# Optimization experiments

Hardware: AMD Instinct MI355X
Metric: run time of the kernel (lower is better)

## Reference

```python
import jax, jax.numpy as jnp
import numpy as np

N_NODES = 50000
N_EDGES = 1600000


def setup_inputs() -> dict:
    key = jax.random.key(0)
    k1, k2, k3, k4 = jax.random.split(key, 4)
    x = jax.random.normal(k1, (N_NODES, 256), dtype=jnp.float32)
    edge_index = jax.random.randint(k2, (2, N_EDGES), 0, N_NODES, dtype=jnp.int64)
    W1 = jax.random.normal(k3, (256, 128), dtype=jnp.float32) * 0.05
    b1 = jnp.zeros((128,), dtype=jnp.float32)
    Wc = jax.random.normal(k4, (128, 10), dtype=jnp.float32) * 0.05
    bc = jnp.zeros((10,), dtype=jnp.float32)
    return {"x": x, "edge_index": edge_index, "W1": W1, "b1": b1,
            "Wc": Wc, "bc": bc, "conv_time": 30}


def reference(x, edge_index, W1, b1, Wc, bc, conv_time):
    """GCNConv(num_features->nhid) with conv_time propagation hops, ReLU, Linear cls."""
    n = x.shape[0]
    # linear transform first (standard GCNConv: transform then propagate)
    h = x @ W1 + b1  # [N, nhid]
    # add self-loops (GCN default)
    loop = jnp.arange(n, dtype=edge_index.dtype)
    src = jnp.concatenate([edge_index[0], loop])
    dst = jnp.concatenate([edge_index[1], loop])
    # symmetric normalization D^{-1/2} A_hat D^{-1/2}
    deg = jax.ops.segment_sum(jnp.ones_like(dst, dtype=h.dtype), dst, num_segments=n)
    dinv = jax.lax.rsqrt(jnp.maximum(deg, 1.0))
    norm = (dinv[src] * dinv[dst])[:, None]  # [E+N, 1]

    def hop(i, h):
        msg = h[src] * norm                      # gather + scale
        return jax.ops.segment_sum(msg, dst, num_segments=n)  # scatter-add

    h = jax.lax.fori_loop(0, conv_time, hop, h)
    h = jax.nn.relu(h)
    return h @ Wc + bc  # [N, num_classes]
```

## Files before the change

### kernel.cpp

```cpp
#include <hip/hip_runtime.h>
#include <hip/hip_bf16.h>

#define NFEAT 256
#define NHID  128
#define NCLS  10
#define CONV_TIME 30
#define NSLICE 8
#define SFEAT  16

__global__ void deg_kernel(const int* __restrict__ ei, int* __restrict__ cnt, int E) {
    int e = blockIdx.x * blockDim.x + threadIdx.x;
    if (e < E) {
        int d = ei[(size_t)E + e];
        atomicAdd(&cnt[d], 1);
    }
}

__global__ void dinv_kernel(const int* __restrict__ cnt, float* __restrict__ dinv, int n) {
    int i = blockIdx.x * blockDim.x + threadIdx.x;
    if (i < n) {
        float deg = (float)(cnt[i] + 1);
        dinv[i] = 1.0f / sqrtf(deg);
    }
}

__global__ void scan_kernel(const int* __restrict__ cnt, int* __restrict__ offs,
                            int* __restrict__ pos, int n) {
    __shared__ int lds[256];
    int tid = threadIdx.x;
    int per = (n + 255) >> 8;
    int beg = tid * per;
    int end = min(beg + per, n);
    int sum = 0;
    for (int i = beg; i < end; ++i) sum += cnt[i];
    lds[tid] = sum;
    __syncthreads();
    if (tid == 0) {
        int acc = 0;
        for (int i = 0; i < 256; ++i) { int t = lds[i]; lds[i] = acc; acc += t; }
    }
    __syncthreads();
    int run = lds[tid];
    for (int i = beg; i < end; ++i) { offs[i] = run; pos[i] = run; run += cnt[i]; }
    if (tid == 255) offs[n] = run;
}

__global__ void scatter_kernel(const int* __restrict__ ei, int* __restrict__ pos,
                               unsigned short* __restrict__ esrc, int E) {
    int e = blockIdx.x * blockDim.x + threadIdx.x;
    if (e < E) {
        int s = ei[e];
        int d = ei[(size_t)E + e];
        int p = atomicAdd(&pos[d], 1);
        esrc[p] = (unsigned short)s;
    }
}

__global__ void init_dummy_kernel(float* __restrict__ hA, float* __restrict__ hB,
                                  int n, int np1) {
    int t = threadIdx.x;
    if (t < NSLICE * SFEAT) {
        int sl = t >> 4, f = t & 15;
        size_t idx = (size_t)sl * np1 * SFEAT + (size_t)n * SFEAT + f;
        hA[idx] = 0.0f;
        hB[idx] = 0.0f;
    }
}

__global__ __launch_bounds__(256) void gemm1_kernel(const float* __restrict__ x,
                                                    const float* __restrict__ W1,
                                                    const float* __restrict__ b1,
                                                    const float* __restrict__ dinv,
                                                    float* __restrict__ g, int M, int np1) {
    __shared__ float As[64][20];
    __shared__ float Bs[16][128];
    int tid = threadIdx.x;
    int m0  = blockIdx.x * 64;
    int tx  = tid & 15;
    int ty  = tid >> 4;
    int ar  = tid >> 2, aq = tid & 3;
    int br  = tid >> 4, bc = tid & 15;

    float acc[4][8];
#pragma unroll
    for (int i = 0; i < 4; ++i)
#pragma unroll
        for (int j = 0; j < 8; ++j) acc[i][j] = 0.0f;

    for (int kb = 0; kb < NFEAT; kb += 16) {
        float4 av = make_float4(0.f, 0.f, 0.f, 0.f);
        int arow = m0 + ar;
        if (arow < M) av = *(const float4*)(x + (size_t)arow * NFEAT + kb + aq * 4);
        *(float4*)&As[ar][aq * 4] = av;
        *(float4*)&Bs[br][bc * 8]     = *(const float4*)(W1 + (size_t)(kb + br) * NHID + bc * 8);
        *(float4*)&Bs[br][bc * 8 + 4] = *(const float4*)(W1 + (size_t)(kb + br) * NHID + bc * 8 + 4);
        __syncthreads();
#pragma unroll
        for (int k = 0; k < 16; ++k) {
            float a0 = As[ty * 4 + 0][k];
            float a1 = As[ty * 4 + 1][k];
            float a2 = As[ty * 4 + 2][k];
            float a3 = As[ty * 4 + 3][k];
            float4 b0 = *(float4*)&Bs[k][tx * 8];
            float4 b1v = *(float4*)&Bs[k][tx * 8 + 4];
            float bv[8] = {b0.x, b0.y, b0.z, b0.w, b1v.x, b1v.y, b1v.z, b1v.w};
            float avv[4] = {a0, a1, a2, a3};
#pragma unroll
            for (int i = 0; i < 4; ++i)
#pragma unroll
                for (int j = 0; j < 8; ++j)
                    acc[i][j] = fmaf(avv[i], bv[j], acc[i][j]);
        }
        __syncthreads();
    }
    int col0 = tx * 8;
    int sl   = col0 >> 4;
    int c0   = col0 & 15;
#pragma unroll
    for (int i = 0; i < 4; ++i) {
        int row = m0 + ty * 4 + i;
        if (row < M) {
            float dv = dinv[row];
            float* dst = g + (size_t)sl * np1 * SFEAT + (size_t)row * SFEAT + c0;
#pragma unroll
            for (int j = 0; j < 8; ++j)
                dst[j] = dv * (acc[i][j] + b1[col0 + j]);
        }
    }
}

__global__ __launch_bounds__(256) void hop_kernel(const float* __restrict__ gin,
                                                  float* __restrict__ gout,
                                                  const int* __restrict__ offs,
                                                  const unsigned short* __restrict__ esrc,
                                                  const float* __restrict__ dinv,
                                                  int n, int np1, int last) {
    int bid  = blockIdx.x;
    int sl   = bid & (NSLICE - 1);
    int grp  = (bid >> 3) * 4 + (threadIdx.x >> 6);
    if (grp * 16 >= n) return;
    int lane = threadIdx.x & 63;
    int slot = lane >> 2;
    int fl   = lane & 3;
    int node = grp * 16 + slot;
    bool valid = node < n;
    int nodeC = valid ? node : n;
    const float4* __restrict__ gs4 = (const float4*)(gin + (size_t)sl * np1 * SFEAT);
    float4*       __restrict__ go4 = (float4*)(gout + (size_t)sl * np1 * SFEAT);

    int beg = 0, deg = 0;
    if (valid) { beg = offs[node]; deg = offs[node + 1] - beg; }
    int dmax = deg;
    dmax = max(dmax, __shfl_xor(dmax, 4, 64));
    dmax = max(dmax, __shfl_xor(dmax, 8, 64));
    dmax = max(dmax, __shfl_xor(dmax, 16, 64));
    dmax = max(dmax, __shfl_xor(dmax, 32, 64));

    float4 acc = make_float4(0.f, 0.f, 0.f, 0.f);
    int degm1 = (deg > 0) ? (deg - 1) : 0;
    for (int i = 0; i < dmax; i += 8) {
#pragma unroll
        for (int j = 0; j < 8; ++j) {
            int a   = beg + min(i + j, degm1);
            int src = (int)esrc[a];
            src     = (i + j < deg) ? src : n;
            float4 v = gs4[(size_t)src * 4 + fl];
            acc.x += v.x; acc.y += v.y; acc.z += v.z; acc.w += v.w;
        }
    }
    float4 sf = gs4[(size_t)nodeC * 4 + fl];
    acc.x += sf.x; acc.y += sf.y; acc.z += sf.z; acc.w += sf.w;
    float dv = valid ? dinv[node] : 1.0f;
    float sc = last ? dv : dv * dv;
    acc.x *= sc; acc.y *= sc; acc.z *= sc; acc.w *= sc;
    if (valid) go4[(size_t)node * 4 + fl] = acc;
}

__global__ __launch_bounds__(256) void cls_kernel(const float* __restrict__ h,
                                                  const float* __restrict__ Wc,
                                                  const float* __restrict__ bc,
                                                  float* __restrict__ out, int n, int np1) {
    __shared__ float wc[NHID * NCLS];
    __shared__ float bcs[NCLS];
    int tid = threadIdx.x;
    for (int i = tid; i < NHID * NCLS; i += 256) wc[i] = Wc[i];
    if (tid < NCLS) bcs[tid] = bc[tid];
    __syncthreads();
    int i = blockIdx.x * 256 + tid;
    if (i >= n) return;
    float acc[NCLS];
#pragma unroll
    for (int c = 0; c < NCLS; ++c) acc[c] = bcs[c];
#pragma unroll
    for (int s = 0; s < NSLICE; ++s) {
        const float4* hr = (const float4*)(h + ((size_t)s * np1 + i) * SFEAT);
#pragma unroll
        for (int q = 0; q < 4; ++q) {
            float4 v = hr[q];
            float vs[4] = {fmaxf(v.x, 0.f), fmaxf(v.y, 0.f), fmaxf(v.z, 0.f), fmaxf(v.w, 0.f)};
#pragma unroll
            for (int j = 0; j < 4; ++j)
#pragma unroll
                for (int c = 0; c < NCLS; ++c)
                    acc[c] = fmaf(vs[j], wc[(s * SFEAT + q * 4 + j) * NCLS + c], acc[c]);
        }
    }
#pragma unroll
    for (int c = 0; c < NCLS; ++c) out[(size_t)i * NCLS + c] = acc[c];
}

static inline size_t align256(size_t x) { return (x + 255) & ~(size_t)255; }

extern "C" void kernel_launch(void* const* d_in, const int* in_sizes, int n_in,
                              void* d_out, int out_size, void* d_ws, size_t ws_size,
                              hipStream_t stream) {
    const float* x   = (const float*)d_in[0];
    const int*   ei  = (const int*)d_in[1];
    const float* W1  = (const float*)d_in[2];
    const float* b1  = (const float*)d_in[3];
    const float* Wc  = (const float*)d_in[4];
    const float* bc  = (const float*)d_in[5];
    float*       out = (float*)d_out;

    const int N   = in_sizes[0] / NFEAT;
    const int E   = in_sizes[1] / 2;
    const int NP1 = N + 1;

    char* ws = (char*)d_ws;
    size_t off = 0;
    float*          hA   = (float*)(ws + off); off = align256(off + (size_t)NSLICE * NP1 * SFEAT * 4);
    float*          hB   = (float*)(ws + off); off = align256(off + (size_t)NSLICE * NP1 * SFEAT * 4);
    int*            cnt  = (int*)  (ws + off); off = align256(off + (size_t)N * 4);
    float*          dinv = (float*)(ws + off); off = align256(off + (size_t)N * 4);
    int*            offs = (int*)  (ws + off); off = align256(off + (size_t)(N + 1) * 4);
    int*            pos  = (int*)  (ws + off); off = align256(off + (size_t)N * 4);
    unsigned short* esrc = (unsigned short*)(ws + off); off = align256(off + ((size_t)E + 64) * 2);

    hipMemsetAsync(cnt, 0, (size_t)N * 4, stream);

    deg_kernel<<<(E + 255) / 256, 256, 0, stream>>>(ei, cnt, E);
    dinv_kernel<<<(N + 255) / 256, 256, 0, stream>>>(cnt, dinv, N);
    scan_kernel<<<1, 256, 0, stream>>>(cnt, offs, pos, N);
    scatter_kernel<<<(E + 255) / 256, 256, 0, stream>>>(ei, pos, esrc, E);
    init_dummy_kernel<<<1, 256, 0, stream>>>(hA, hB, N, NP1);

    gemm1_kernel<<<(N + 63) / 64, 256, 0, stream>>>(x, W1, b1, dinv, hA, N, NP1);

    int ngrp = (N + 15) / 16;
    int hop_blocks = NSLICE * ((ngrp + 3) / 4);
    for (int i = 0; i < CONV_TIME; ++i) {
        const float* gi = (i & 1) ? hB : hA;
        float*       go = (i & 1) ? hA : hB;
        hop_kernel<<<hop_blocks, 256, 0, stream>>>(gi, go, offs, esrc, dinv, N, NP1,
                                                   (i == CONV_TIME - 1) ? 1 : 0);
    }

    cls_kernel<<<(N + 255) / 256, 256, 0, stream>>>(hA, Wc, bc, out, N, NP1);
}
```

Baseline: 2.658 ms.

## Pad per-node edge lists to multiples of eight and load indices as uint4

```diff
diff --git a/kernel.cpp b/kernel.cpp
--- a/kernel.cpp
+++ b/kernel.cpp
@@ -24,25 +24,35 @@
     }
 }
 
-__global__ void scan_kernel(const int* __restrict__ cnt, int* __restrict__ offs,
-                            int* __restrict__ pos, int n) {
-    __shared__ int lds[256];
-    int tid = threadIdx.x;
-    int per = (n + 255) >> 8;
-    int beg = tid * per;
-    int end = min(beg + per, n);
-    int sum = 0;
-    for (int i = beg; i < end; ++i) sum += cnt[i];
-    lds[tid] = sum;
-    __syncthreads();
-    if (tid == 0) {
-        int acc = 0;
-        for (int i = 0; i < 256; ++i) { int t = lds[i]; lds[i] = acc; acc += t; }
-    }
-    __syncthreads();
-    int run = lds[tid];
-    for (int i = beg; i < end; ++i) { offs[i] = run; pos[i] = run; run += cnt[i]; }
-    if (tid == 255) offs[n] = run;
+__global__ void alloc_kernel(const int* __restrict__ cnt, int* __restrict__ alloc,
+                             int* __restrict__ pbeg, int* __restrict__ plen,
+                             int* __restrict__ pos, int n) {
+    int i    = blockIdx.x * blockDim.x + threadIdx.x;
+    int lane = threadIdx.x & 63;
+    int pl   = 0;
+    if (i < n) pl = (cnt[i] + 7) & ~7;
+    int v = pl;
+#pragma unroll
+    for (int d = 1; d < 64; d <<= 1) {
+        int t = __shfl_up(v, d, 64);
+        if (lane >= d) v += t;
+    }
+    int total = __shfl(v, 63, 64);
+    int excl  = v - pl;
+    int base  = 0;
+    if (lane == 63) base = atomicAdd(alloc, total);
+    base = __shfl(base, 63, 64);
+    if (i < n) {
+        int seg = base + excl;
+        pbeg[i] = seg;
+        plen[i] = pl;
+        pos[i]  = seg;
+    }
+}
+
+__global__ void fill_esrc_kernel(unsigned int* __restrict__ esrc32, unsigned int val, int nwords) {
+    int i = blockIdx.x * blockDim.x + threadIdx.x;
+    if (i < nwords) esrc32[i] = val;
 }
 
 __global__ void scatter_kernel(const int* __restrict__ ei, int* __restrict__ pos,
@@ -131,7 +141,8 @@
 
 __global__ __launch_bounds__(256) void hop_kernel(const float* __restrict__ gin,
                                                   float* __restrict__ gout,
-                                                  const int* __restrict__ offs,
+                                                  const int* __restrict__ pbeg,
+                                                  const int* __restrict__ plen,
                                                   const unsigned short* __restrict__ esrc,
                                                   const float* __restrict__ dinv,
                                                   int n, int np1, int last) {
@@ -148,25 +159,29 @@
     const float4* __restrict__ gs4 = (const float4*)(gin + (size_t)sl * np1 * SFEAT);
     float4*       __restrict__ go4 = (float4*)(gout + (size_t)sl * np1 * SFEAT);
 
-    int beg = 0, deg = 0;
-    if (valid) { beg = offs[node]; deg = offs[node + 1] - beg; }
-    int dmax = deg;
-    dmax = max(dmax, __shfl_xor(dmax, 4, 64));
-    dmax = max(dmax, __shfl_xor(dmax, 8, 64));
-    dmax = max(dmax, __shfl_xor(dmax, 16, 64));
-    dmax = max(dmax, __shfl_xor(dmax, 32, 64));
+    int beg = 0, L = 0;
+    if (valid) { beg = pbeg[node]; L = plen[node]; }
 
     float4 acc = make_float4(0.f, 0.f, 0.f, 0.f);
-    int degm1 = (deg > 0) ? (deg - 1) : 0;
-    for (int i = 0; i < dmax; i += 8) {
-#pragma unroll
-        for (int j = 0; j < 8; ++j) {
-            int a   = beg + min(i + j, degm1);
-            int src = (int)esrc[a];
-            src     = (i + j < deg) ? src : n;
-            float4 v = gs4[(size_t)src * 4 + fl];
-            acc.x += v.x; acc.y += v.y; acc.z += v.z; acc.w += v.w;
-        }
+    const uint4* __restrict__ e4 = (const uint4*)esrc;
+    for (int i = 0; i < L; i += 8) {
+        uint4 w = e4[(beg + i) >> 3];
+        int s0 = w.x & 0xFFFF, s1 = w.x >> 16;
+        int s2 = w.y & 0xFFFF, s3 = w.y >> 16;
+        int s4 = w.z & 0xFFFF, s5 = w.z >> 16;
+        int s6 = w.w & 0xFFFF, s7 = w.w >> 16;
+        float4 v0 = gs4[(size_t)s0 * 4 + fl];
+        float4 v1 = gs4[(size_t)s1 * 4 + fl];
+        float4 v2 = gs4[(size_t)s2 * 4 + fl];
+        float4 v3 = gs4[(size_t)s3 * 4 + fl];
+        float4 v4 = gs4[(size_t)s4 * 4 + fl];
+        float4 v5 = gs4[(size_t)s5 * 4 + fl];
+        float4 v6 = gs4[(size_t)s6 * 4 + fl];
+        float4 v7 = gs4[(size_t)s7 * 4 + fl];
+        acc.x += v0.x + v1.x + v2.x + v3.x + v4.x + v5.x + v6.x + v7.x;
+        acc.y += v0.y + v1.y + v2.y + v3.y + v4.y + v5.y + v6.y + v7.y;
+        acc.z += v0.z + v1.z + v2.z + v3.z + v4.z + v5.z + v6.z + v7.z;
+        acc.w += v0.w + v1.w + v2.w + v3.w + v4.w + v5.w + v6.w + v7.w;
     }
     float4 sf = gs4[(size_t)nodeC * 4 + fl];
     acc.x += sf.x; acc.y += sf.y; acc.z += sf.z; acc.w += sf.w;
@@ -222,25 +237,33 @@
     const float* bc  = (const float*)d_in[5];
     float*       out = (float*)d_out;
 
-    const int N   = in_sizes[0] / NFEAT;
-    const int E   = in_sizes[1] / 2;
-    const int NP1 = N + 1;
+    const int N    = in_sizes[0] / NFEAT;
+    const int E    = in_sizes[1] / 2;
+    const int NP1  = N + 1;
+    const int EPAD = E + 8 * N + 64;
 
     char* ws = (char*)d_ws;
     size_t off = 0;
     float*          hA   = (float*)(ws + off); off = align256(off + (size_t)NSLICE * NP1 * SFEAT * 4);
     float*          hB   = (float*)(ws + off); off = align256(off + (size_t)NSLICE * NP1 * SFEAT * 4);
-    int*            cnt  = (int*)  (ws + off); off = align256(off + (size_t)N * 4);
+    int*            cnt  = (int*)  (ws + off); off = align256(off + (size_t)(N + 64) * 4);
     float*          dinv = (float*)(ws + off); off = align256(off + (size_t)N * 4);
-    int*            offs = (int*)  (ws + off); off = align256(off + (size_t)(N + 1) * 4);
+    int*            pbeg = (int*)  (ws + off); off = align256(off + (size_t)N * 4);
+    int*            plen = (int*)  (ws + off); off = align256(off + (size_t)N * 4);
     int*            pos  = (int*)  (ws + off); off = align256(off + (size_t)N * 4);
-    unsigned short* esrc = (unsigned short*)(ws + off); off = align256(off + ((size_t)E + 64) * 2);
-
-    hipMemsetAsync(cnt, 0, (size_t)N * 4, stream);
+    unsigned short* esrc = (unsigned short*)(ws + off); off = align256(off + (size_t)EPAD * 2);
+    int*            alloc = cnt + N;
+
+    hipMemsetAsync(cnt, 0, (size_t)(N + 64) * 4, stream);
 
     deg_kernel<<<(E + 255) / 256, 256, 0, stream>>>(ei, cnt, E);
     dinv_kernel<<<(N + 255) / 256, 256, 0, stream>>>(cnt, dinv, N);
-    scan_kernel<<<1, 256, 0, stream>>>(cnt, offs, pos, N);
+    alloc_kernel<<<(N + 255) / 256, 256, 0, stream>>>(cnt, alloc, pbeg, plen, pos, N);
+    {
+        unsigned int v = ((unsigned)N << 16) | (unsigned)N;
+        int nwords = EPAD / 2;
+        fill_esrc_kernel<<<(nwords + 255) / 256, 256, 0, stream>>>((unsigned int*)esrc, v, nwords);
+    }
     scatter_kernel<<<(E + 255) / 256, 256, 0, stream>>>(ei, pos, esrc, E);
     init_dummy_kernel<<<1, 256, 0, stream>>>(hA, hB, N, NP1);
 
@@ -251,7 +274,7 @@
     for (int i = 0; i < CONV_TIME; ++i) {
         const float* gi = (i & 1) ? hB : hA;
         float*       go = (i & 1) ? hA : hB;
-        hop_kernel<<<hop_blocks, 256, 0, stream>>>(gi, go, offs, esrc, dinv, N, NP1,
+        hop_kernel<<<hop_blocks, 256, 0, stream>>>(gi, go, pbeg, plen, esrc, dinv, N, NP1,
                                                    (i == CONV_TIME - 1) ? 1 : 0);
     }
 
```

Measured after the change: 2.446 ms. 1.09x faster.
